# Kernel optimization log

Measured on AMD Instinct MI355X. Metric: run time of the kernel, lower is better.

## Reference

```python
import jax, jax.numpy as jnp
import numpy as np

N = 40000   # nodes
E = 640000  # edges (avg degree 16)
D = 128     # in_dim
G = 64      # graphs in batch
C = 100     # n_classes
L = 3       # hidden_layers + 1 AGNN layers
EPS = 1e-12 # F.normalize eps


def setup_inputs() -> dict:
    key = jax.random.key(0)
    ks = jax.random.split(key, 6)
    h = jax.random.normal(ks[0], (N, D), jnp.float32)
    src = jax.random.randint(ks[1], (E,), 0, N, jnp.int32)
    dst = jax.random.randint(ks[2], (E,), 0, N, jnp.int32)
    graph_ids = jnp.sort(jax.random.randint(ks[3], (N,), 0, G, jnp.int32))
    betas = jnp.ones((L,), jnp.float32)  # init_beta=1.0, one learnable beta per AGNNConv
    W_cls = jax.random.normal(ks[4], (D, C), jnp.float32) / np.sqrt(D)
    b_cls = jnp.zeros((C,), jnp.float32)
    return dict(h=h, src=src, dst=dst, graph_ids=graph_ids,
                betas=betas, W_cls=W_cls, b_cls=b_cls)


def agnn_layer(h, src, dst, beta):
    # cosine-similarity attention (DGL AGNNConv)
    nh = h / (jnp.linalg.norm(h, axis=-1, keepdims=True) + EPS)  # [N, D]
    s = beta * jnp.sum(nh[src] * nh[dst], axis=-1)               # [E] edge scores
    # segment softmax over incoming edges of each dst node
    m = jax.ops.segment_max(s, dst, num_segments=N)              # [N]
    m = jnp.where(jnp.isfinite(m), m, 0.0)                       # empty segments -> 0
    a = jnp.exp(s - m[dst])                                      # [E]
    denom = jax.ops.segment_sum(a, dst, num_segments=N)          # [N]
    num = jax.ops.segment_sum(a[:, None] * h[src], dst, num_segments=N)  # [N, D]
    return num / jnp.where(denom > 0, denom, 1.0)[:, None]


def reference(h, src, dst, graph_ids, betas, W_cls, b_cls):
    # dropout is identity at inference; batch_norms are unused in the original forward
    for l in range(L):
        h = agnn_layer(h, src, dst, betas[l])
    # AvgPooling readout: per-graph mean of node features
    hg = jax.ops.segment_sum(h, graph_ids, num_segments=G)       # [G, D]
    cnt = jax.ops.segment_sum(jnp.ones((N,), h.dtype), graph_ids, num_segments=G)
    hg = hg / jnp.maximum(cnt, 1.0)[:, None]
    return hg @ W_cls + b_cls                                    # [G, C]
```

## Files before the change

### kernel.cpp

```cpp
#include <hip/hip_runtime.h>
#include <hip/hip_fp16.h>
#include <math.h>

#define N_NODES 40000
#define N_EDGES 640000
#define DIM     128
#define N_GRAPHS 64
#define N_CLS   100
#define N_LAYERS 3
#define EPSN    1e-12f


__global__ void k_zero_int(int* __restrict__ a, int n) {
    int i = blockIdx.x * blockDim.x + threadIdx.x;
    if (i < n) a[i] = 0;
}

__global__ void k_count(const int* __restrict__ dst, int* __restrict__ counts) {
    int e = blockIdx.x * blockDim.x + threadIdx.x;
    if (e < N_EDGES) atomicAdd(&counts[dst[e]], 1);
}

#define SCAN_T 1024
#define SCAN_V 40
__global__ void k_scan(const int* __restrict__ counts, int* __restrict__ offsets) {
    __shared__ int lds[SCAN_T];
    int t = threadIdx.x;
    int base = t * SCAN_V;
    int tsum = 0;
    if (base < N_NODES) {
        for (int k = 0; k < SCAN_V; ++k) tsum += counts[base + k];
    }
    lds[t] = tsum; __syncthreads();
    int x = tsum;
    for (int off = 1; off < SCAN_T; off <<= 1) {
        int y = (t >= off) ? lds[t - off] : 0;
        __syncthreads();
        x += y;
        lds[t] = x;
        __syncthreads();
    }
    int excl = x - tsum;
    if (base < N_NODES) {
        int run = excl;
        for (int k = 0; k < SCAN_V; ++k) {
            offsets[base + k] = run;
            run += counts[base + k];
        }
    }
    if (t == (N_NODES / SCAN_V)) offsets[N_NODES] = excl;
}

__global__ void k_scatter(const int* __restrict__ src, const int* __restrict__ dst,
                          const int* __restrict__ offsets, int* __restrict__ cursor,
                          int* __restrict__ csr_src) {
    int e = blockIdx.x * blockDim.x + threadIdx.x;
    if (e >= N_EDGES) return;
    int d = dst[e];
    int p = offsets[d] + atomicAdd(&cursor[d], 1);
    csr_src[p] = src[e];
}


__global__ void k_norm(const float* __restrict__ h, float* __restrict__ inv,
                       __half2* __restrict__ hh) {
    int node = (blockIdx.x * blockDim.x + threadIdx.x) >> 6;
    int lane = threadIdx.x & 63;
    if (node >= N_NODES) return;
    const float2* r2 = (const float2*)(h + (size_t)node * DIM);
    float2 v = r2[lane];
    float ss = v.x * v.x + v.y * v.y;
    #pragma unroll
    for (int o = 32; o; o >>= 1) ss += __shfl_xor(ss, o);
    if (lane == 0) inv[node] = 1.0f / (sqrtf(ss) + EPSN);
    hh[(size_t)node * 64 + lane] = __floats2half2_rn(v.x, v.y);
}

union H8 { int4 i4; __half2 h2[4]; };

__device__ __forceinline__ void cvt8(const H8& u, float* f) {
    #pragma unroll
    for (int k = 0; k < 4; ++k) {
        float2 v = __half22float2(u.h2[k]);
        f[2 * k]     = v.x;
        f[2 * k + 1] = v.y;
    }
}

template <bool LAST>
__global__ void k_fused(const int4* __restrict__ hh_in,
                        const float* __restrict__ inv_in,
                        const int* __restrict__ csr_src,
                        const int* __restrict__ offsets,
                        const float* __restrict__ betas, int layer,
                        int4* __restrict__ hh_out,
                        float* __restrict__ h_out_f32,
                        float* __restrict__ inv_out) {
    int node = (blockIdx.x * blockDim.x + threadIdx.x) >> 6;
    int lane = threadIdx.x & 63;
    if (node >= N_NODES) return;
    int grp = lane >> 4;
    int t   = lane & 15;

    int off = offsets[node];
    int deg = offsets[node + 1] - off;

    size_t nrow16 = (size_t)node * 16;
    H8 selfu; selfu.i4 = hh_in[nrow16 + t];
    float hd[8]; cvt8(selfu, hd);
    float bi = betas[layer] * inv_in[node];

    float dsum = 0.f;
    float ac[8];
    #pragma unroll
    for (int k = 0; k < 8; ++k) ac[k] = 0.f;

    if (deg > 0) {
        int last = deg - 1;
        int jb = 0;
        for (; jb + 8 <= deg; jb += 8) {
            int s0 = csr_src[off + jb + grp];
            int s1 = csr_src[off + jb + 4 + grp];
            H8 u0, u1;
            u0.i4 = hh_in[(size_t)s0 * 16 + t];
            u1.i4 = hh_in[(size_t)s1 * 16 + t];
            float iv0 = inv_in[s0], iv1 = inv_in[s1];
            float f0[8], f1[8];
            cvt8(u0, f0); cvt8(u1, f1);
            float p0 = 0.f, p1 = 0.f;
            #pragma unroll
            for (int k = 0; k < 8; ++k) { p0 += f0[k] * hd[k]; p1 += f1[k] * hd[k]; }
            #pragma unroll
            for (int o = 8; o; o >>= 1) {
                p0 += __shfl_xor(p0, o);
                p1 += __shfl_xor(p1, o);
            }
            float w0 = __expf(bi * iv0 * p0);
            float w1 = __expf(bi * iv1 * p1);
            dsum += w0 + w1;
            #pragma unroll
            for (int k = 0; k < 8; ++k) ac[k] += w0 * f0[k] + w1 * f1[k];
        }
        for (; jb < deg; jb += 4) {
            int j = jb + grp;
            bool valid = j <= last;
            int idx = valid ? j : last;
            int s = csr_src[off + idx];
            H8 u; u.i4 = hh_in[(size_t)s * 16 + t];
            float iv = inv_in[s];
            float f[8]; cvt8(u, f);
            float p = 0.f;
            #pragma unroll
            for (int k = 0; k < 8; ++k) p += f[k] * hd[k];
            #pragma unroll
            for (int o = 8; o; o >>= 1) p += __shfl_xor(p, o);
            float w = valid ? __expf(bi * iv * p) : 0.f;
            dsum += w;
            #pragma unroll
            for (int k = 0; k < 8; ++k) ac[k] += w * f[k];
        }

        #pragma unroll
        for (int o = 16; o < 64; o <<= 1) {
            dsum += __shfl_xor(dsum, o);
            #pragma unroll
            for (int k = 0; k < 8; ++k) ac[k] += __shfl_xor(ac[k], o);
        }
        float invd = 1.0f / dsum;
        #pragma unroll
        for (int k = 0; k < 8; ++k) ac[k] *= invd;
    }

    if (LAST) {
        if (grp == 0) {
            float4* o4 = (float4*)(h_out_f32 + (size_t)node * DIM);
            o4[2 * t]     = make_float4(ac[0], ac[1], ac[2], ac[3]);
            o4[2 * t + 1] = make_float4(ac[4], ac[5], ac[6], ac[7]);
        }
    } else {
        if (grp == 0) {
            H8 w;
            #pragma unroll
            for (int k = 0; k < 4; ++k)
                w.h2[k] = __floats2half2_rn(ac[2 * k], ac[2 * k + 1]);
            hh_out[nrow16 + t] = w.i4;
        }
        float ss = 0.f;
        #pragma unroll
        for (int k = 0; k < 8; ++k) ss += ac[k] * ac[k];
        #pragma unroll
        for (int o = 8; o; o >>= 1) ss += __shfl_xor(ss, o);
        if (lane == 0) inv_out[node] = 1.0f / (sqrtf(ss) + EPSN);
    }
}


#define POOL_BLOCKS 640
__global__ void k_pool_partial(const float* __restrict__ h, const int* __restrict__ gid,
                               float* __restrict__ hgsum, int* __restrict__ gcount) {
    int nPer = (N_NODES + gridDim.x - 1) / gridDim.x;
    int n0 = blockIdx.x * nPer;
    int n1 = n0 + nPer; if (n1 > N_NODES) n1 = N_NODES;
    if (n0 >= n1) return;
    int c = threadIdx.x;
    int curg = gid[n0];
    int segstart = n0;
    float acc = 0.f;
    for (int n = n0; n < n1; ++n) {
        int g = gid[n];
        if (g != curg) {
            atomicAdd(&hgsum[curg * DIM + c], acc);
            if (c == 0) atomicAdd(&gcount[curg], n - segstart);
            acc = 0.f; curg = g; segstart = n;
        }
        acc += h[(size_t)n * DIM + c];
    }
    atomicAdd(&hgsum[curg * DIM + c], acc);
    if (c == 0) atomicAdd(&gcount[curg], n1 - segstart);
}

__global__ void k_cls(const float* __restrict__ hgsum, const int* __restrict__ gcount,
                      const float* __restrict__ W, const float* __restrict__ b,
                      float* __restrict__ out) {
    int g = blockIdx.x;
    int c = threadIdx.x;
    if (c >= N_CLS) return;
    float invc = 1.0f / fmaxf((float)gcount[g], 1.0f);
    float acc = 0.f;
    #pragma unroll 8
    for (int d = 0; d < DIM; ++d) acc += hgsum[g * DIM + d] * W[d * N_CLS + c];
    out[g * N_CLS + c] = b[c] + acc * invc;
}


extern "C" void kernel_launch(void* const* d_in, const int* in_sizes, int n_in,
                              void* d_out, int out_size, void* d_ws, size_t ws_size,
                              hipStream_t stream) {
    const float* h_in  = (const float*)d_in[0];
    const int*   src   = (const int*)  d_in[1];
    const int*   dst   = (const int*)  d_in[2];
    const int*   gid   = (const int*)  d_in[3];
    const float* betas = (const float*)d_in[4];
    const float* W     = (const float*)d_in[5];
    const float* bcls  = (const float*)d_in[6];
    float* out = (float*)d_out;

    char* p = (char*)d_ws;
    int4*  hh0     = (int4*)p;  p += (size_t)N_NODES * DIM * 2;
    int4*  hh1     = (int4*)p;  p += (size_t)N_NODES * DIM * 2;
    float* hf32    = (float*)p; p += (size_t)N_NODES * DIM * 4;
    float* inv0    = (float*)p; p += (size_t)N_NODES * 4;
    float* inv1    = (float*)p; p += (size_t)N_NODES * 4;
    int*   counts  = (int*)p;   p += (size_t)N_NODES * 4;
    int*   cursor  = (int*)p;   p += (size_t)N_NODES * 4;
    float* hgsum   = (float*)p; p += (size_t)N_GRAPHS * DIM * 4;
    int*   gcount  = (int*)p;   p += (size_t)N_GRAPHS * 4;
    int*   offsets = (int*)p;   p += (size_t)(N_NODES + 4) * 4;
    int*   csr_src = (int*)p;   p += (size_t)N_EDGES * 4;

    const int ZERO_N = 2 * N_NODES + N_GRAPHS * DIM + N_GRAPHS;

    k_zero_int<<<(ZERO_N + 255) / 256, 256, 0, stream>>>(counts, ZERO_N);
    k_count<<<(N_EDGES + 255) / 256, 256, 0, stream>>>(dst, counts);
    k_scan<<<1, SCAN_T, 0, stream>>>(counts, offsets);
    k_scatter<<<(N_EDGES + 255) / 256, 256, 0, stream>>>(src, dst, offsets, cursor, csr_src);

    k_norm<<<N_NODES / 4, 256, 0, stream>>>(h_in, inv0, (__half2*)hh0);
    k_fused<false><<<N_NODES / 4, 256, 0, stream>>>(hh0, inv0, csr_src, offsets, betas, 0,
                                                    hh1, nullptr, inv1);
    k_fused<false><<<N_NODES / 4, 256, 0, stream>>>(hh1, inv1, csr_src, offsets, betas, 1,
                                                    hh0, nullptr, inv0);
    k_fused<true><<<N_NODES / 4, 256, 0, stream>>>(hh0, inv0, csr_src, offsets, betas, 2,
                                                   nullptr, hf32, inv1);

    k_pool_partial<<<POOL_BLOCKS, DIM, 0, stream>>>(hf32, gid, hgsum, gcount);
    k_cls<<<N_GRAPHS, DIM, 0, stream>>>(hgsum, gcount, W, bcls, out);
}
```

Before: 213.3 us.

## Fuse mean pooling into last AGNN layer and drop scatter cursor atomics

The last layer now accumulates each node's output straight into per-graph sums, first in shared memory when all four nodes in a block share a graph, otherwise with global atomics. This removes the float32 hidden-state write and the separate pooling kernel. Per-graph node counts are found by binary search over the sorted graph ids inside the classifier kernel. The CSR build records each edge's slot from the counting atomic, so the scatter pass needs no second atomic. The cost is more global atomics on hgsum, whose float summation order is not deterministic.

```diff
diff --git a/kernel.cpp b/kernel.cpp
--- a/kernel.cpp
+++ b/kernel.cpp
@@ -16,9 +16,10 @@
     if (i < n) a[i] = 0;
 }
 
-__global__ void k_count(const int* __restrict__ dst, int* __restrict__ counts) {
+__global__ void k_count(const int* __restrict__ dst, int* __restrict__ counts,
+                        int* __restrict__ posw) {
     int e = blockIdx.x * blockDim.x + threadIdx.x;
-    if (e < N_EDGES) atomicAdd(&counts[dst[e]], 1);
+    if (e < N_EDGES) posw[e] = atomicAdd(&counts[dst[e]], 1);
 }
 
 #define SCAN_T 1024
@@ -52,13 +53,11 @@
 }
 
 __global__ void k_scatter(const int* __restrict__ src, const int* __restrict__ dst,
-                          const int* __restrict__ offsets, int* __restrict__ cursor,
+                          const int* __restrict__ offsets, const int* __restrict__ posw,
                           int* __restrict__ csr_src) {
     int e = blockIdx.x * blockDim.x + threadIdx.x;
     if (e >= N_EDGES) return;
-    int d = dst[e];
-    int p = offsets[d] + atomicAdd(&cursor[d], 1);
-    csr_src[p] = src[e];
+    csr_src[offsets[dst[e]] + posw[e]] = src[e];
 }
 
 
@@ -94,11 +93,11 @@
                         const int* __restrict__ offsets,
                         const float* __restrict__ betas, int layer,
                         int4* __restrict__ hh_out,
-                        float* __restrict__ h_out_f32,
-                        float* __restrict__ inv_out) {
+                        float* __restrict__ inv_out,
+                        const int* __restrict__ gid,
+                        float* __restrict__ hgsum) {
     int node = (blockIdx.x * blockDim.x + threadIdx.x) >> 6;
     int lane = threadIdx.x & 63;
-    if (node >= N_NODES) return;
     int grp = lane >> 4;
     int t   = lane & 15;
 
@@ -172,10 +171,27 @@
     }
 
     if (LAST) {
-        if (grp == 0) {
-            float4* o4 = (float4*)(h_out_f32 + (size_t)node * DIM);
-            o4[2 * t]     = make_float4(ac[0], ac[1], ac[2], ac[3]);
-            o4[2 * t + 1] = make_float4(ac[4], ac[5], ac[6], ac[7]);
+        __shared__ float spool[DIM];
+        __shared__ int sg[4];
+        int tid = threadIdx.x;
+        int g = gid[node];
+        if (lane == 0) sg[tid >> 6] = g;
+        if (tid < DIM) spool[tid] = 0.f;
+        __syncthreads();
+        bool uni = (sg[0] == sg[1]) && (sg[1] == sg[2]) && (sg[2] == sg[3]);
+        if (uni) {
+            if (grp == 0) {
+                #pragma unroll
+                for (int k = 0; k < 8; ++k) atomicAdd(&spool[8 * t + k], ac[k]);
+            }
+            __syncthreads();
+            if (tid < DIM) atomicAdd(&hgsum[(size_t)sg[0] * DIM + tid], spool[tid]);
+        } else {
+            if (grp == 0) {
+                #pragma unroll
+                for (int k = 0; k < 8; ++k)
+                    atomicAdd(&hgsum[(size_t)g * DIM + 8 * t + k], ac[k]);
+            }
         }
     } else {
         if (grp == 0) {
@@ -195,41 +211,26 @@
 }
 
 
-#define POOL_BLOCKS 640
-__global__ void k_pool_partial(const float* __restrict__ h, const int* __restrict__ gid,
-                               float* __restrict__ hgsum, int* __restrict__ gcount) {
-    int nPer = (N_NODES + gridDim.x - 1) / gridDim.x;
-    int n0 = blockIdx.x * nPer;
-    int n1 = n0 + nPer; if (n1 > N_NODES) n1 = N_NODES;
-    if (n0 >= n1) return;
-    int c = threadIdx.x;
-    int curg = gid[n0];
-    int segstart = n0;
-    float acc = 0.f;
-    for (int n = n0; n < n1; ++n) {
-        int g = gid[n];
-        if (g != curg) {
-            atomicAdd(&hgsum[curg * DIM + c], acc);
-            if (c == 0) atomicAdd(&gcount[curg], n - segstart);
-            acc = 0.f; curg = g; segstart = n;
-        }
-        acc += h[(size_t)n * DIM + c];
-    }
-    atomicAdd(&hgsum[curg * DIM + c], acc);
-    if (c == 0) atomicAdd(&gcount[curg], n1 - segstart);
-}
-
-__global__ void k_cls(const float* __restrict__ hgsum, const int* __restrict__ gcount,
+__global__ void k_cls(const float* __restrict__ hgsum, const int* __restrict__ gid,
                       const float* __restrict__ W, const float* __restrict__ b,
                       float* __restrict__ out) {
     int g = blockIdx.x;
     int c = threadIdx.x;
+    __shared__ float invc_s;
+    if (c == 0) {
+        int lo = 0, hi = N_NODES;
+        while (lo < hi) { int mid = (lo + hi) >> 1; if (gid[mid] < g) lo = mid + 1; else hi = mid; }
+        int start = lo;
+        lo = 0; hi = N_NODES;
+        while (lo < hi) { int mid = (lo + hi) >> 1; if (gid[mid] < g + 1) lo = mid + 1; else hi = mid; }
+        invc_s = 1.0f / fmaxf((float)(lo - start), 1.0f);
+    }
+    __syncthreads();
     if (c >= N_CLS) return;
-    float invc = 1.0f / fmaxf((float)gcount[g], 1.0f);
     float acc = 0.f;
     #pragma unroll 8
     for (int d = 0; d < DIM; ++d) acc += hgsum[g * DIM + d] * W[d * N_CLS + c];
-    out[g * N_CLS + c] = b[c] + acc * invc;
+    out[g * N_CLS + c] = b[c] + acc * invc_s;
 }
 
 
@@ -248,31 +249,28 @@
     char* p = (char*)d_ws;
     int4*  hh0     = (int4*)p;  p += (size_t)N_NODES * DIM * 2;
     int4*  hh1     = (int4*)p;  p += (size_t)N_NODES * DIM * 2;
-    float* hf32    = (float*)p; p += (size_t)N_NODES * DIM * 4;
     float* inv0    = (float*)p; p += (size_t)N_NODES * 4;
     float* inv1    = (float*)p; p += (size_t)N_NODES * 4;
     int*   counts  = (int*)p;   p += (size_t)N_NODES * 4;
-    int*   cursor  = (int*)p;   p += (size_t)N_NODES * 4;
     float* hgsum   = (float*)p; p += (size_t)N_GRAPHS * DIM * 4;
-    int*   gcount  = (int*)p;   p += (size_t)N_GRAPHS * 4;
     int*   offsets = (int*)p;   p += (size_t)(N_NODES + 4) * 4;
+    int*   posw    = (int*)p;   p += (size_t)N_EDGES * 4;
     int*   csr_src = (int*)p;   p += (size_t)N_EDGES * 4;
 
-    const int ZERO_N = 2 * N_NODES + N_GRAPHS * DIM + N_GRAPHS;
+    const int ZERO_N = N_NODES + N_GRAPHS * DIM;
 
     k_zero_int<<<(ZERO_N + 255) / 256, 256, 0, stream>>>(counts, ZERO_N);
-    k_count<<<(N_EDGES + 255) / 256, 256, 0, stream>>>(dst, counts);
+    k_count<<<(N_EDGES + 255) / 256, 256, 0, stream>>>(dst, counts, posw);
     k_scan<<<1, SCAN_T, 0, stream>>>(counts, offsets);
-    k_scatter<<<(N_EDGES + 255) / 256, 256, 0, stream>>>(src, dst, offsets, cursor, csr_src);
+    k_scatter<<<(N_EDGES + 255) / 256, 256, 0, stream>>>(src, dst, offsets, posw, csr_src);
 
     k_norm<<<N_NODES / 4, 256, 0, stream>>>(h_in, inv0, (__half2*)hh0);
     k_fused<false><<<N_NODES / 4, 256, 0, stream>>>(hh0, inv0, csr_src, offsets, betas, 0,
-                                                    hh1, nullptr, inv1);
+                                                    hh1, inv1, nullptr, nullptr);
     k_fused<false><<<N_NODES / 4, 256, 0, stream>>>(hh1, inv1, csr_src, offsets, betas, 1,
-                                                    hh0, nullptr, inv0);
+                                                    hh0, inv0, nullptr, nullptr);
     k_fused<true><<<N_NODES / 4, 256, 0, stream>>>(hh0, inv0, csr_src, offsets, betas, 2,
-                                                   nullptr, hf32, inv1);
-
-    k_pool_partial<<<POOL_BLOCKS, DIM, 0, stream>>>(hf32, gid, hgsum, gcount);
-    k_cls<<<N_GRAPHS, DIM, 0, stream>>>(hgsum, gcount, W, bcls, out);
-}
+                                                   nullptr, nullptr, gid, hgsum);
+
+    k_cls<<<N_GRAPHS, DIM, 0, stream>>>(hgsum, gid, W, bcls, out);
+}
```

Measured after the change: 200.6 us. 6.0% less time.
